# Kernel tuning notes

Hardware: AMD Instinct MI355X
Metric: run time of the kernel (lower is better)

The kernel has to match this reference:

```python
import jax, jax.numpy as jnp
import numpy as np

MAX_SEQLEN = 2048  # static max sequence length (flash varlen APIs take this as a host arg)


def setup_inputs() -> dict:
    key = jax.random.key(0)
    k1, k2, k3 = jax.random.split(key, 3)
    T, H, D = 8192, 8, 128
    B = 4
    q = jax.random.normal(k1, (T, H, D), dtype=jnp.float32)
    k = jax.random.normal(k2, (T, H, D), dtype=jnp.float32)
    v = jax.random.normal(k3, (T, H, D), dtype=jnp.float32)
    cu = (jnp.arange(B + 1, dtype=jnp.int32) * (T // B))  # [0,2048,4096,6144,8192]
    return {"q": q, "k": k, "v": v, "cu_seqlens_q": cu, "cu_seqlens_k": cu}


def reference(q, k, v, cu_seqlens_q, cu_seqlens_k):
    """Varlen (ragged) multi-head attention, non-causal (flash_attn varlen default).

    q,k,v: [T, H, D] packed over sequences; cu_seqlens: [B+1] boundaries.
    Gathers each sequence into a padded [B, S, H, D] layout, computes
    per-sequence softmax(q k^T / sqrt(D)) v with padding masked, then
    scatters back to packed [T, H, D].
    """
    T, H, D = q.shape
    B = cu_seqlens_q.shape[0] - 1
    S = MAX_SEQLEN
    scale = 1.0 / jnp.sqrt(jnp.asarray(D, q.dtype))

    pos = jnp.arange(S)
    q_start = cu_seqlens_q[:-1]
    k_start = cu_seqlens_k[:-1]
    q_len = jnp.diff(cu_seqlens_q)  # [B]
    k_len = jnp.diff(cu_seqlens_k)

    q_idx = jnp.clip(q_start[:, None] + pos[None, :], 0, T - 1)  # [B, S]
    k_idx = jnp.clip(k_start[:, None] + pos[None, :], 0, T - 1)
    q_valid = pos[None, :] < q_len[:, None]  # [B, S]
    k_valid = pos[None, :] < k_len[:, None]

    qb = q[q_idx]  # [B, S, H, D]
    kb = k[k_idx]
    vb = v[k_idx]

    scores = jnp.einsum('bqhd,bkhd->bhqk', qb, kb) * scale  # [B, H, S, S]
    neg = jnp.asarray(-1e30, scores.dtype)
    scores = jnp.where(k_valid[:, None, None, :], scores, neg)
    attn = jax.nn.softmax(scores, axis=-1)
    ob = jnp.einsum('bhqk,bkhd->bqhd', attn, vb)  # [B, S, H, D]

    # zero padded query rows, then scatter-add back to packed layout
    ob = jnp.where(q_valid[:, :, None, None], ob, 0.0)
    out = jnp.zeros_like(q).at[q_idx.reshape(-1)].add(ob.reshape(B * S, H, D))
    return out
```

## Files before the change

kernel.cpp:

```cpp
#include <hip/hip_runtime.h>
#include <hip/hip_bf16.h>
#include <stdint.h>

#define HH 8
#define DD 128
#define MAXSEQ 2048
#define QBLK 128

typedef float f32x16 __attribute__((ext_vector_type(16)));
typedef short s16x8 __attribute__((ext_vector_type(8)));

__device__ __forceinline__ unsigned short f2bf(float x) {
  union { float f; uint32_t u; } v; v.f = x;
  uint32_t u = v.u;
  return (unsigned short)((u + 0x7FFFu + ((u >> 16) & 1u)) >> 16);
}

__device__ __forceinline__ void gload_lds16(const unsigned short* g, unsigned short* l) {
  __builtin_amdgcn_global_load_lds((const __attribute__((address_space(1))) void*)g,
                                   (__attribute__((address_space(3))) void*)l, 16, 0, 0);
}

__global__ void zero_rows(const int* __restrict__ cuq, float* __restrict__ out, int T, int B) {
  const int t = blockIdx.x * blockDim.x + threadIdx.x;
  if (t >= T) return;
  bool covered = false;
  for (int b = 0; b < B; ++b) {
    const int s = cuq[b];
    const int len = min(cuq[b + 1] - s, MAXSEQ);
    if (t >= s && t < s + len) covered = true;
  }
  if (!covered) {
    float4* p = (float4*)(out + (size_t)t * HH * DD);
#pragma unroll 4
    for (int i = 0; i < HH * DD / 4; ++i) p[i] = float4{0.f, 0.f, 0.f, 0.f};
  }
}

__global__ void kvconv(const float* __restrict__ k, const float* __restrict__ v,
                       unsigned short* __restrict__ kb2, unsigned short* __restrict__ vb2, int T) {
  const int TBc = T >> 5;
  const int total = TBc * HH * 512;
  int u = blockIdx.x * blockDim.x + threadIdx.x;
  if (u < total) {
    const int lp = u & 63;
    const int key = lp & 31, hi = lp >> 5;
    int r = u >> 6;
    const int c = r & 7; r >>= 3;
    const int tb = r % TBc;
    const int h = r / TBc;
    const int t = tb * 32 + key;
    const int d = c * 16 + hi * 8;
    const float* src = k + ((size_t)t * HH + h) * DD + d;
    float4 a = *(const float4*)src;
    float4 cc = *(const float4*)(src + 4);
    union { unsigned short us[8]; uint4 q; } w;
    w.us[0] = f2bf(a.x); w.us[1] = f2bf(a.y); w.us[2] = f2bf(a.z); w.us[3] = f2bf(a.w);
    w.us[4] = f2bf(cc.x); w.us[5] = f2bf(cc.y); w.us[6] = f2bf(cc.z); w.us[7] = f2bf(cc.w);
    *(uint4*)(kb2 + (size_t)u * 8) = w.q;
  } else if ((u -= total) < total) {
    const int lo = u & 31;
    const int hi = (u >> 5) & 1;
    const int i = (u >> 6) & 7;
    const int dt = i & 3, ks2 = i >> 2;
    int r = u >> 9;
    const int tb = r % TBc;
    const int h = r / TBc;
    const int d = dt * 32 + lo;
    union { unsigned short us[8]; uint4 q; } w;
#pragma unroll
    for (int j = 0; j < 8; ++j) {
      const int phys = 16 * ks2 + ((j < 4) ? (4 * hi + j) : (8 + 4 * hi + (j - 4)));
      const int t = tb * 32 + phys;
      w.us[j] = f2bf(v[((size_t)t * HH + h) * DD + d]);
    }
    *(uint4*)(vb2 + (size_t)u * 8) = w.q;
  }
}

__global__ __launch_bounds__(256, 2)
void attn_main(const float* __restrict__ q,
               const unsigned short* __restrict__ kb2,
               const unsigned short* __restrict__ vb2,
               const int* __restrict__ cuq,
               const int* __restrict__ cuk,
               float* __restrict__ out,
               int T, int BH) {
  extern __shared__ __align__(16) unsigned short smem[];

  const int TBc = T >> 5;
  const int bid = blockIdx.x;
  const int bh = bid % BH;
  const int qt = bid / BH;
  const int b = bh / HH, h = bh % HH;
  const int qs = cuq[b], qe = cuq[b + 1];
  const int ks = cuk[b], ke = cuk[b + 1];
  const int nq = min(qe - qs, MAXSEQ);
  const int nk = min(ke - ks, MAXSEQ);
  if (qt * QBLK >= nq || nk <= 0) return;

  const int tid = threadIdx.x;
  const int wave = tid >> 6;
  const int lane = tid & 63;
  const int lo = lane & 31;
  const int hi = lane >> 5;
  const int wub = (tid & ~63) * 8;

  const int kb32 = ks >> 5;
  const unsigned short* kb2h = kb2 + (size_t)h * TBc * 4096;
  const unsigned short* vb2h = vb2 + (size_t)h * TBc * 4096;

  const float SC = (1.0f / 11.313708498984761f) * 1.4426950408889634f;
  const int qrow = qt * QBLK + wave * 32 + lo;
  const int qg = qs + min(qrow, nq - 1);
  const float* qp = q + ((size_t)qg * HH + h) * DD;
  s16x8 qf[8];
#pragma unroll
  for (int c = 0; c < 8; ++c) {
    const float* p0 = qp + c * 16 + hi * 8;
    float4 a = *(const float4*)(p0);
    float4 cc = *(const float4*)(p0 + 4);
    union { unsigned short us[8]; s16x8 v; } u;
    u.us[0] = f2bf(a.x * SC); u.us[1] = f2bf(a.y * SC);
    u.us[2] = f2bf(a.z * SC); u.us[3] = f2bf(a.w * SC);
    u.us[4] = f2bf(cc.x * SC); u.us[5] = f2bf(cc.y * SC);
    u.us[6] = f2bf(cc.z * SC); u.us[7] = f2bf(cc.w * SC);
    qf[c] = u.v;
  }

  f32x16 Oa[4];
#pragma unroll
  for (int i = 0; i < 4; ++i)
#pragma unroll
    for (int r = 0; r < 16; ++r) Oa[i][r] = 0.0f;

  float l_run = 0.0f;
  const int nkt = (nk + 63) / 64;

  auto stageK = [&](int buf, int kt) {
    unsigned short* Kd = smem + buf * 8192;
#pragma unroll
    for (int r = 0; r < 4; ++r) {
      const int u = r * 256 + tid;
      const int tb = min(kb32 + 2 * kt + (u >> 9), TBc - 1);
      gload_lds16(kb2h + (size_t)tb * 4096 + (size_t)(u & 511) * 8, Kd + (size_t)(r * 256) * 8 + wub);
    }
  };

  stageK(0, 0);
  __syncthreads();

  int buf = 0;
  for (int kt = 0; kt < nkt; ++kt) {
    s16x8 vfA[8];
    {
      const size_t base = (size_t)min(kb32 + 2 * kt, TBc - 1) * 4096;
#pragma unroll
      for (int i = 0; i < 8; ++i) vfA[i] = *(const s16x8*)(vb2h + base + i * 512 + lane * 8);
    }

    if (kt + 1 < nkt) stageK(buf ^ 1, kt + 1);

    const unsigned short* Kb = smem + buf * 8192;

    f32x16 st0, st1;
#pragma unroll
    for (int r = 0; r < 16; ++r) { st0[r] = 0.0f; st1[r] = 0.0f; }
    {
      s16x8 kfA[8];
#pragma unroll
      for (int c = 0; c < 8; ++c) kfA[c] = *(const s16x8*)(Kb + c * 512 + lane * 8);
      __builtin_amdgcn_s_setprio(1);
#pragma unroll
      for (int c = 0; c < 8; ++c)
        st0 = __builtin_amdgcn_mfma_f32_32x32x16_bf16(kfA[c], qf[c], st0, 0, 0, 0);
      __builtin_amdgcn_s_setprio(0);
    }
    {
      s16x8 kfB[8];
#pragma unroll
      for (int c = 0; c < 8; ++c) kfB[c] = *(const s16x8*)(Kb + 4096 + c * 512 + lane * 8);
      __builtin_amdgcn_s_setprio(1);
#pragma unroll
      for (int c = 0; c < 8; ++c)
        st1 = __builtin_amdgcn_mfma_f32_32x32x16_bf16(kfB[c], qf[c], st1, 0, 0, 0);
      __builtin_amdgcn_s_setprio(0);
    }

    s16x8 vfB[8];
    {
      const size_t base = (size_t)min(kb32 + 2 * kt + 1, TBc - 1) * 4096;
#pragma unroll
      for (int i = 0; i < 8; ++i) vfB[i] = *(const s16x8*)(vb2h + base + i * 512 + lane * 8);
    }

    const int lim = nk - kt * 64;
    if (lim < 64) {
#pragma unroll
      for (int r = 0; r < 16; ++r) {
        const int a = (r & 3) + 8 * (r >> 2) + 4 * hi;
        if (a >= lim) st0[r] = -__builtin_inff();
        if (a + 32 >= lim) st1[r] = -__builtin_inff();
      }
    }

    float p[32];
#pragma unroll
    for (int r = 0; r < 16; ++r) {
      p[r] = __builtin_amdgcn_exp2f(st0[r]);
      p[16 + r] = __builtin_amdgcn_exp2f(st1[r]);
    }
    float ps = 0.f;
#pragma unroll
    for (int r = 0; r < 32; r += 4) ps += (p[r] + p[r + 1]) + (p[r + 2] + p[r + 3]);
    l_run += ps;

    uint32_t pw[16];
#pragma unroll
    for (int g = 0; g < 8; ++g) {
      uint32_t w0, w1;
      asm("v_cvt_pk_bf16_f32 %0, %1, %2" : "=v"(w0) : "v"(p[4 * g + 0]), "v"(p[4 * g + 1]));
      asm("v_cvt_pk_bf16_f32 %0, %1, %2" : "=v"(w1) : "v"(p[4 * g + 2]), "v"(p[4 * g + 3]));
      pw[2 * g] = w0;
      pw[2 * g + 1] = w1;
    }

    __builtin_amdgcn_s_setprio(1);
#pragma unroll
    for (int ks2 = 0; ks2 < 2; ++ks2) {
      union { uint32_t u[4]; s16x8 v; } pa;
      pa.u[0] = pw[4 * ks2 + 0]; pa.u[1] = pw[4 * ks2 + 1];
      pa.u[2] = pw[4 * ks2 + 2]; pa.u[3] = pw[4 * ks2 + 3];
#pragma unroll
      for (int dt = 0; dt < 4; ++dt)
        Oa[dt] = __builtin_amdgcn_mfma_f32_32x32x16_bf16(pa.v, vfA[ks2 * 4 + dt], Oa[dt], 0, 0, 0);
    }
#pragma unroll
    for (int ks2 = 0; ks2 < 2; ++ks2) {
      union { uint32_t u[4]; s16x8 v; } pa;
      pa.u[0] = pw[8 + 4 * ks2 + 0]; pa.u[1] = pw[8 + 4 * ks2 + 1];
      pa.u[2] = pw[8 + 4 * ks2 + 2]; pa.u[3] = pw[8 + 4 * ks2 + 3];
#pragma unroll
      for (int dt = 0; dt < 4; ++dt)
        Oa[dt] = __builtin_amdgcn_mfma_f32_32x32x16_bf16(pa.v, vfB[ks2 * 4 + dt], Oa[dt], 0, 0, 0);
    }
    __builtin_amdgcn_s_setprio(0);

    if (kt + 1 < nkt) {
      __syncthreads();
      buf ^= 1;
    }
  }

  l_run += __shfl_xor(l_run, 32);
  const float linv = 1.0f / l_run;
#pragma unroll
  for (int r = 0; r < 16; ++r) {
    const int src = (r & 3) + 8 * (r >> 2) + 4 * hi;
    const float li = __shfl(linv, src);
    const int qirow = qt * QBLK + wave * 32 + src;
    if (qirow < nq) {
      float* op = out + ((size_t)(qs + qirow) * HH + h) * DD;
      op[0 * 32 + lo] = Oa[0][r] * li;
      op[1 * 32 + lo] = Oa[1][r] * li;
      op[2 * 32 + lo] = Oa[2][r] * li;
      op[3 * 32 + lo] = Oa[3][r] * li;
    }
  }
}

extern "C" void kernel_launch(void* const* d_in, const int* in_sizes, int n_in,
                              void* d_out, int out_size, void* d_ws, size_t ws_size,
                              hipStream_t stream) {
  const float* q = (const float*)d_in[0];
  const float* k = (const float*)d_in[1];
  const float* v = (const float*)d_in[2];
  const int* cuq = (const int*)d_in[3];
  const int* cuk = (const int*)d_in[4];
  float* out = (float*)d_out;
  const int T = in_sizes[0] / (HH * DD);
  const int B = in_sizes[3] - 1;

  unsigned short* kb2 = (unsigned short*)d_ws;
  unsigned short* vb2 = kb2 + (size_t)T * HH * DD;
  const size_t need = (size_t)T * HH * DD * 2 * 2;
  if (ws_size < need) return;

  {
    zero_rows<<<(T + 255) / 256, 256, 0, stream>>>(cuq, out, T, B);
  }
  {
    const int total = (T >> 5) * HH * 512;
    kvconv<<<(2 * total + 255) / 256, 256, 0, stream>>>(k, v, kb2, vb2, T);
  }
  {
    const int BH = B * HH;
    const int scap = MAXSEQ < T ? MAXSEQ : T;
    const int qtiles = (scap + QBLK - 1) / QBLK;
    attn_main<<<BH * qtiles, 256, 32768, stream>>>(q, kb2, vb2, cuq, cuk, out, T, BH);
  }
}
```

Before: 110.3 us.

## Split KV range across wave pairs with 64-row Q tiles and LDS reduction

Halves the query tile to 64 rows and assigns the four waves as 2 query groups by 2 KV halves, so each wave processes half the keys (32-key tiles) and partial outputs are combined through LDS at the end. This doubles the grid size and raises the occupancy target to 3 blocks per CU to fill the GPU better. The trade-off is an extra LDS reduction and sync at the end, smaller MFMA work per iteration, and K/V reuse across query rows is halved. Without max subtraction the partial sums combine directly, but correctness assumes nk <= 2048.

After: 124.1 us. 12.5% more time.

```diff
diff --git a/kernel.cpp b/kernel.cpp
--- a/kernel.cpp
+++ b/kernel.cpp
@@ -5,7 +5,7 @@
 #define HH 8
 #define DD 128
 #define MAXSEQ 2048
-#define QBLK 128
+#define QBLK 64
 
 typedef float f32x16 __attribute__((ext_vector_type(16)));
 typedef short s16x8 __attribute__((ext_vector_type(8)));
@@ -78,7 +78,7 @@
   }
 }
 
-__global__ __launch_bounds__(256, 2)
+__global__ __launch_bounds__(256, 3)
 void attn_main(const float* __restrict__ q,
                const unsigned short* __restrict__ kb2,
                const unsigned short* __restrict__ vb2,
@@ -104,14 +104,15 @@
   const int lane = tid & 63;
   const int lo = lane & 31;
   const int hi = lane >> 5;
-  const int wub = (tid & ~63) * 8;
+  const int wq = wave & 1;
+  const int wk = wave >> 1;
 
   const int kb32 = ks >> 5;
   const unsigned short* kb2h = kb2 + (size_t)h * TBc * 4096;
   const unsigned short* vb2h = vb2 + (size_t)h * TBc * 4096;
 
   const float SC = (1.0f / 11.313708498984761f) * 1.4426950408889634f;
-  const int qrow = qt * QBLK + wave * 32 + lo;
+  const int qrow = qt * QBLK + wq * 32 + lo;
   const int qg = qs + min(qrow, nq - 1);
   const float* qp = q + ((size_t)qg * HH + h) * DD;
   s16x8 qf[8];
@@ -135,15 +136,20 @@
     for (int r = 0; r < 16; ++r) Oa[i][r] = 0.0f;
 
   float l_run = 0.0f;
-  const int nkt = (nk + 63) / 64;
+
+  const int len_wk = min(nk - wk * 1024, 1024);
+  const int myT = len_wk > 0 ? (len_wk + 31) / 32 : 0;
+  const int nkt = (min(nk, 1024) + 31) / 32;
+  const int tb0 = kb32 + wk * 32;
 
   auto stageK = [&](int buf, int kt) {
-    unsigned short* Kd = smem + buf * 8192;
 #pragma unroll
     for (int r = 0; r < 4; ++r) {
-      const int u = r * 256 + tid;
-      const int tb = min(kb32 + 2 * kt + (u >> 9), TBc - 1);
-      gload_lds16(kb2h + (size_t)tb * 4096 + (size_t)(u & 511) * 8, Kd + (size_t)(r * 256) * 8 + wub);
+      const int half = r >> 1;
+      const int tb = min(kb32 + half * 32 + kt, TBc - 1);
+      const int ul = (r & 1) * 256 + tid;
+      gload_lds16(kb2h + (size_t)tb * 4096 + (size_t)ul * 8,
+                  smem + (size_t)(half * 2 + buf) * 4096 + (size_t)((r & 1) * 256 + (tid & ~63)) * 8);
     }
   };
 
@@ -152,99 +158,82 @@
 
   int buf = 0;
   for (int kt = 0; kt < nkt; ++kt) {
-    s16x8 vfA[8];
-    {
-      const size_t base = (size_t)min(kb32 + 2 * kt, TBc - 1) * 4096;
-#pragma unroll
-      for (int i = 0; i < 8; ++i) vfA[i] = *(const s16x8*)(vb2h + base + i * 512 + lane * 8);
-    }
-
     if (kt + 1 < nkt) stageK(buf ^ 1, kt + 1);
 
-    const unsigned short* Kb = smem + buf * 8192;
-
-    f32x16 st0, st1;
-#pragma unroll
-    for (int r = 0; r < 16; ++r) { st0[r] = 0.0f; st1[r] = 0.0f; }
-    {
-      s16x8 kfA[8];
-#pragma unroll
-      for (int c = 0; c < 8; ++c) kfA[c] = *(const s16x8*)(Kb + c * 512 + lane * 8);
+    if (kt < myT) {
+      const unsigned short* Kslot = smem + (size_t)(wk * 2 + buf) * 4096;
+      const int tb = min(tb0 + kt, TBc - 1);
+
+      f32x16 st;
+#pragma unroll
+      for (int r = 0; r < 16; ++r) st[r] = 0.0f;
+      {
+        s16x8 kf[8];
+#pragma unroll
+        for (int c = 0; c < 8; ++c) kf[c] = *(const s16x8*)(Kslot + c * 512 + lane * 8);
+        __builtin_amdgcn_s_setprio(1);
+#pragma unroll
+        for (int c = 0; c < 8; ++c)
+          st = __builtin_amdgcn_mfma_f32_32x32x16_bf16(kf[c], qf[c], st, 0, 0, 0);
+        __builtin_amdgcn_s_setprio(0);
+      }
+
+      s16x8 vfA[4];
+#pragma unroll
+      for (int i = 0; i < 4; ++i)
+        vfA[i] = *(const s16x8*)(vb2h + (size_t)tb * 4096 + i * 512 + lane * 8);
+
+      const int lim = len_wk - kt * 32;
+      if (lim < 32) {
+#pragma unroll
+        for (int r = 0; r < 16; ++r) {
+          const int a = (r & 3) + 8 * (r >> 2) + 4 * hi;
+          if (a >= lim) st[r] = -__builtin_inff();
+        }
+      }
+
+      float p[16];
+#pragma unroll
+      for (int r = 0; r < 16; ++r) p[r] = __builtin_amdgcn_exp2f(st[r]);
+      float ps = 0.f;
+#pragma unroll
+      for (int r = 0; r < 16; r += 4) ps += (p[r] + p[r + 1]) + (p[r + 2] + p[r + 3]);
+      l_run += ps;
+
+      uint32_t pw[8];
+#pragma unroll
+      for (int g = 0; g < 4; ++g) {
+        uint32_t w0, w1;
+        asm("v_cvt_pk_bf16_f32 %0, %1, %2" : "=v"(w0) : "v"(p[4 * g + 0]), "v"(p[4 * g + 1]));
+        asm("v_cvt_pk_bf16_f32 %0, %1, %2" : "=v"(w1) : "v"(p[4 * g + 2]), "v"(p[4 * g + 3]));
+        pw[2 * g] = w0;
+        pw[2 * g + 1] = w1;
+      }
+
       __builtin_amdgcn_s_setprio(1);
-#pragma unroll
-      for (int c = 0; c < 8; ++c)
-        st0 = __builtin_amdgcn_mfma_f32_32x32x16_bf16(kfA[c], qf[c], st0, 0, 0, 0);
+      {
+        union { uint32_t u[4]; s16x8 v; } pa;
+        pa.u[0] = pw[0]; pa.u[1] = pw[1]; pa.u[2] = pw[2]; pa.u[3] = pw[3];
+#pragma unroll
+        for (int dt = 0; dt < 4; ++dt)
+          Oa[dt] = __builtin_amdgcn_mfma_f32_32x32x16_bf16(pa.v, vfA[dt], Oa[dt], 0, 0, 0);
+      }
       __builtin_amdgcn_s_setprio(0);
-    }
-    {
-      s16x8 kfB[8];
-#pragma unroll
-      for (int c = 0; c < 8; ++c) kfB[c] = *(const s16x8*)(Kb + 4096 + c * 512 + lane * 8);
+
+      s16x8 vfB[4];
+#pragma unroll
+      for (int i = 0; i < 4; ++i)
+        vfB[i] = *(const s16x8*)(vb2h + (size_t)tb * 4096 + (4 + i) * 512 + lane * 8);
       __builtin_amdgcn_s_setprio(1);
-#pragma unroll
-      for (int c = 0; c < 8; ++c)
-        st1 = __builtin_amdgcn_mfma_f32_32x32x16_bf16(kfB[c], qf[c], st1, 0, 0, 0);
+      {
+        union { uint32_t u[4]; s16x8 v; } pa;
+        pa.u[0] = pw[4]; pa.u[1] = pw[5]; pa.u[2] = pw[6]; pa.u[3] = pw[7];
+#pragma unroll
+        for (int dt = 0; dt < 4; ++dt)
+          Oa[dt] = __builtin_amdgcn_mfma_f32_32x32x16_bf16(pa.v, vfB[dt], Oa[dt], 0, 0, 0);
+      }
       __builtin_amdgcn_s_setprio(0);
     }
-
-    s16x8 vfB[8];
-    {
-      const size_t base = (size_t)min(kb32 + 2 * kt + 1, TBc - 1) * 4096;
-#pragma unroll
-      for (int i = 0; i < 8; ++i) vfB[i] = *(const s16x8*)(vb2h + base + i * 512 + lane * 8);
-    }
-
-    const int lim = nk - kt * 64;
-    if (lim < 64) {
-#pragma unroll
-      for (int r = 0; r < 16; ++r) {
-        const int a = (r & 3) + 8 * (r >> 2) + 4 * hi;
-        if (a >= lim) st0[r] = -__builtin_inff();
-        if (a + 32 >= lim) st1[r] = -__builtin_inff();
-      }
-    }
-
-    float p[32];
-#pragma unroll
-    for (int r = 0; r < 16; ++r) {
-      p[r] = __builtin_amdgcn_exp2f(st0[r]);
-      p[16 + r] = __builtin_amdgcn_exp2f(st1[r]);
-    }
-    float ps = 0.f;
-#pragma unroll
-    for (int r = 0; r < 32; r += 4) ps += (p[r] + p[r + 1]) + (p[r + 2] + p[r + 3]);
-    l_run += ps;
-
-    uint32_t pw[16];
-#pragma unroll
-    for (int g = 0; g < 8; ++g) {
-      uint32_t w0, w1;
-      asm("v_cvt_pk_bf16_f32 %0, %1, %2" : "=v"(w0) : "v"(p[4 * g + 0]), "v"(p[4 * g + 1]));
-      asm("v_cvt_pk_bf16_f32 %0, %1, %2" : "=v"(w1) : "v"(p[4 * g + 2]), "v"(p[4 * g + 3]));
-      pw[2 * g] = w0;
-      pw[2 * g + 1] = w1;
-    }
-
-    __builtin_amdgcn_s_setprio(1);
-#pragma unroll
-    for (int ks2 = 0; ks2 < 2; ++ks2) {
-      union { uint32_t u[4]; s16x8 v; } pa;
-      pa.u[0] = pw[4 * ks2 + 0]; pa.u[1] = pw[4 * ks2 + 1];
-      pa.u[2] = pw[4 * ks2 + 2]; pa.u[3] = pw[4 * ks2 + 3];
-#pragma unroll
-      for (int dt = 0; dt < 4; ++dt)
-        Oa[dt] = __builtin_amdgcn_mfma_f32_32x32x16_bf16(pa.v, vfA[ks2 * 4 + dt], Oa[dt], 0, 0, 0);
-    }
-#pragma unroll
-    for (int ks2 = 0; ks2 < 2; ++ks2) {
-      union { uint32_t u[4]; s16x8 v; } pa;
-      pa.u[0] = pw[8 + 4 * ks2 + 0]; pa.u[1] = pw[8 + 4 * ks2 + 1];
-      pa.u[2] = pw[8 + 4 * ks2 + 2]; pa.u[3] = pw[8 + 4 * ks2 + 3];
-#pragma unroll
-      for (int dt = 0; dt < 4; ++dt)
-        Oa[dt] = __builtin_amdgcn_mfma_f32_32x32x16_bf16(pa.v, vfB[ks2 * 4 + dt], Oa[dt], 0, 0, 0);
-    }
-    __builtin_amdgcn_s_setprio(0);
 
     if (kt + 1 < nkt) {
       __syncthreads();
@@ -253,18 +242,38 @@
   }
 
   l_run += __shfl_xor(l_run, 32);
-  const float linv = 1.0f / l_run;
-#pragma unroll
-  for (int r = 0; r < 16; ++r) {
-    const int src = (r & 3) + 8 * (r >> 2) + 4 * hi;
-    const float li = __shfl(linv, src);
-    const int qirow = qt * QBLK + wave * 32 + src;
-    if (qirow < nq) {
-      float* op = out + ((size_t)(qs + qirow) * HH + h) * DD;
-      op[0 * 32 + lo] = Oa[0][r] * li;
-      op[1 * 32 + lo] = Oa[1][r] * li;
-      op[2 * 32 + lo] = Oa[2][r] * li;
-      op[3 * 32 + lo] = Oa[3][r] * li;
+  float* fbuf = (float*)smem;
+  float* lbuf = fbuf + 8192;
+  __syncthreads();
+  if (wk == 1) {
+#pragma unroll
+    for (int r = 0; r < 16; ++r) {
+      const int src = (r & 3) + 8 * (r >> 2) + 4 * hi;
+      float* row = fbuf + (size_t)wq * 4096 + (size_t)src * 128;
+      row[0 * 32 + lo] = Oa[0][r];
+      row[1 * 32 + lo] = Oa[1][r];
+      row[2 * 32 + lo] = Oa[2][r];
+      row[3 * 32 + lo] = Oa[3][r];
+    }
+    if (hi == 0) lbuf[wq * 32 + lo] = l_run;
+  }
+  __syncthreads();
+  if (wk == 0) {
+    const float l_tot = l_run + lbuf[wq * 32 + lo];
+    const float linv = 1.0f / l_tot;
+#pragma unroll
+    for (int r = 0; r < 16; ++r) {
+      const int src = (r & 3) + 8 * (r >> 2) + 4 * hi;
+      const float li = __shfl(linv, src);
+      const int qirow = qt * QBLK + wq * 32 + src;
+      if (qirow < nq) {
+        const float* row = fbuf + (size_t)wq * 4096 + (size_t)src * 128;
+        float* op = out + ((size_t)(qs + qirow) * HH + h) * DD;
+        op[0 * 32 + lo] = (Oa[0][r] + row[0 * 32 + lo]) * li;
+        op[1 * 32 + lo] = (Oa[1][r] + row[1 * 32 + lo]) * li;
+        op[2 * 32 + lo] = (Oa[2][r] + row[2 * 32 + lo]) * li;
+        op[3 * 32 + lo] = (Oa[3][r] + row[3 * 32 + lo]) * li;
+      }
     }
   }
 }
@@ -297,6 +306,6 @@
     const int BH = B * HH;
     const int scap = MAXSEQ < T ? MAXSEQ : T;
     const int qtiles = (scap + QBLK - 1) / QBLK;
-    attn_main<<<BH * qtiles, 256, 32768, stream>>>(q, kb2, vb2, cuq, cuk, out, T, BH);
-  }
-}
+    attn_main<<<BH * qtiles, 256, 33280, stream>>>(q, kb2, vb2, cuq, cuk, out, T, BH);
+  }
+}
```
